# Performance work log

Hardware: AMD Instinct MI355X
Metric: run time of the kernel (lower is better)

## Reference

```python
import jax, jax.numpy as jnp
import numpy as np

B, C, N, HID, OUT = 32768, 128, 12, 200, 2
POOL = 3  # MaxPool2d((1,3), stride=(1,1)) -> N-2 = 10 outputs
EPS = 1e-5


def setup_inputs() -> dict:
    key = jax.random.key(0)
    ks = jax.random.split(key, 18)
    s = 0.05
    return {
        "x": jax.random.normal(ks[0], (B, C, 1, N), jnp.float32),
        "wq": jax.random.normal(ks[1], (C, C), jnp.float32) * s,
        "bq": jax.random.normal(ks[2], (C,), jnp.float32) * s,
        "wk": jax.random.normal(ks[3], (C, C), jnp.float32) * s,
        "bk": jax.random.normal(ks[4], (C,), jnp.float32) * s,
        "wv": jax.random.normal(ks[5], (C, C), jnp.float32) * s,
        "bv": jax.random.normal(ks[6], (C,), jnp.float32) * s,
        "rel_h": jax.random.normal(ks[7], (1, C, N, 1), jnp.float32),
        "rel_w": jax.random.normal(ks[8], (1, C, 1, 1), jnp.float32),
        "bn_gamma": jax.random.uniform(ks[9], (C,), jnp.float32, 0.5, 1.5),
        "bn_beta": jax.random.normal(ks[10], (C,), jnp.float32) * s,
        "bn_mean": jax.random.normal(ks[11], (C,), jnp.float32) * s,
        "bn_var": jax.random.uniform(ks[12], (C,), jnp.float32, 0.5, 1.5),
        "fc1_w": jax.random.normal(ks[13], (HID, (N - POOL + 1) * C), jnp.float32) * s,
        "fc1_b": jax.random.normal(ks[14], (HID,), jnp.float32) * s,
        "fc2_w": jax.random.normal(ks[15], (OUT, HID), jnp.float32) * s,
        "fc2_b": jax.random.normal(ks[16], (OUT,), jnp.float32) * s,
    }


def reference(x, wq, bq, wk, bk, wv, bv, rel_h, rel_w,
              bn_gamma, bn_beta, bn_mean, bn_var,
              fc1_w, fc1_b, fc2_w, fc2_b):
    b, c, w, h = x.shape  # [B, C, 1, 12]
    n = w * h
    xf = x.reshape(b, c, n)  # flatten spatial
    # 1x1 convs == per-position channel mixing
    q = jnp.einsum('oc,bcn->bon', wq, xf) + bq[None, :, None]
    k = jnp.einsum('oc,bcn->bon', wk, xf) + bk[None, :, None]
    v = jnp.einsum('oc,bcn->bon', wv, xf) + bv[None, :, None]
    # content-content: q^T k -> [B, N, N]
    cc = jnp.einsum('bcn,bcm->bnm', q, k)
    # relative-position bias: pos^T q -> [B, N, N]
    pos = (rel_h + rel_w).reshape(c, n)
    cp = jnp.einsum('cn,bcm->bnm', pos, q)
    attn = jax.nn.softmax(cc + cp, axis=-1)
    # out = v @ attn^T : out[b,c,m] = sum_n v[b,c,n] * attn[b,m,n]
    out = jnp.einsum('bcn,bmn->bcm', v, attn)  # [B, C, N]
    # BatchNorm2d (inference) + ReLU
    inv = bn_gamma / jnp.sqrt(bn_var + EPS)
    out = jax.nn.relu(out * inv[None, :, None] + (bn_beta - bn_mean * inv)[None, :, None])
    # MaxPool2d (1,3) stride (1,1) along the N axis
    m = n - POOL + 1
    pooled = jnp.max(jnp.stack([out[..., i:i + m] for i in range(POOL)], axis=0), axis=0)  # [B, C, 10]
    flat = pooled.reshape(b, -1)  # matches torch .view(B,-1) C-major order
    hid = jax.nn.relu(flat @ fc1_w.T + fc1_b)  # dropout = identity (eval)
    return jax.nn.sigmoid(hid @ fc2_w.T + fc2_b)
```

## Files before the change

kernel.cpp:

```cpp
#include <hip/hip_runtime.h>
#include <hip/hip_bf16.h>

#define OFF_G    0u
#define OFF_WVT  32768u
#define OFF_RT   65536u
#define OFF_BNS  71680u
#define OFF_BNB  72192u
#define OFF_FLAG 72704u
#define OFF_W1   72768u
#define OFF_P    605248u

typedef __attribute__((ext_vector_type(8))) unsigned short ushort8_t;
typedef __attribute__((ext_vector_type(8))) __bf16 bf16x8;
typedef __attribute__((ext_vector_type(4))) float f32x4;

static __device__ __forceinline__ float bfbits2f(unsigned short u) {
    return __uint_as_float(((unsigned)u) << 16);
}
static __device__ __forceinline__ unsigned short f2bfbits(float f) {
    __hip_bfloat16 h = __float2bfloat16(f);
    return *(unsigned short*)&h;
}
static __device__ __forceinline__ unsigned pack2bf(float a, float b) {
    return (unsigned)f2bfbits(a) | ((unsigned)f2bfbits(b) << 16);
}
static __device__ __forceinline__ f32x4 mfma16x16x32(ushort8_t a, ushort8_t b, f32x4 c) {
    return __builtin_amdgcn_mfma_f32_16x16x32_bf16(
        __builtin_bit_cast(bf16x8, a), __builtin_bit_cast(bf16x8, b), c, 0, 0, 0);
}

__global__ void setup_kernel(const float* __restrict__ wq, const float* __restrict__ bq,
                             const float* __restrict__ wk,
                             const float* __restrict__ rel_h, const float* __restrict__ rel_w,
                             const float* __restrict__ wv, const float* __restrict__ bvp,
                             const float* __restrict__ gamma, const float* __restrict__ beta,
                             const float* __restrict__ mean, const float* __restrict__ var,
                             const float* __restrict__ fc1w,
                             char* __restrict__ ws)
{
    __hip_bfloat16* GA  = (__hip_bfloat16*)(ws + OFF_G);
    __hip_bfloat16* WA  = (__hip_bfloat16*)(ws + OFF_WVT);
    float*          Rm  = (float*)(ws + OFF_RT);
    float*          BnS = (float*)(ws + OFF_BNS);
    float*          Bi2 = (float*)(ws + OFF_BNB);
    __hip_bfloat16* W1  = (__hip_bfloat16*)(ws + OFF_W1);

    int idx = blockIdx.x * blockDim.x + threadIdx.x;
    if (idx < 16384) {
        int c = idx >> 7, a = idx & 127;
        float s = 0.f;
        for (int o = 0; o < 128; ++o) s += wq[o * 128 + a] * wk[o * 128 + c];
        GA[idx] = __float2bfloat16(s);
    } else if (idx < 32768) {
        int t = idx - 16384;
        int oc = t >> 7;
        float inv = gamma[oc] * rsqrtf(var[oc] + 1e-5f);
        WA[t] = __float2bfloat16(wv[t] * inv);
    } else if (idx < 34304) {
        int t = idx - 32768;
        int c = t / 12, i = t - c * 12;
        float s = 0.f;
        for (int o = 0; o < 128; ++o)
            s += bq[o] * wk[o * 128 + c] + wq[o * 128 + c] * (rel_h[o * 12 + i] + rel_w[o]);
        Rm[t] = s;
    } else if (idx < 34432) {
        int c = idx - 34304;
        float inv = gamma[c] * rsqrtf(var[c] + 1e-5f);
        BnS[c] = inv;
        Bi2[c] = bvp[c] * inv + beta[c] - mean[c] * inv;
    } else if (idx < 300672) {
        int t = idx - 34432;
        int h = t / 1280, k = t - h * 1280;
        W1[t] = (h < 200) ? __float2bfloat16(fc1w[h * 1280 + k])
                          : __float2bfloat16(0.f);
    } else if (idx < 300736) {
        int l = idx - 300672;
        int m = l & 15, g = l >> 4;
        ushort8_t av, bv8;
        for (int j = 0; j < 8; ++j) {
            int k = g * 8 + j;
            float aval = (float)(((m * 5 + k * 3) % 7) - 3);
            float bval = (float)(((k * 11 + m * 2) % 5) - 2);
            av[j]  = (unsigned short)(__float_as_uint(aval) >> 16);
            bv8[j] = (unsigned short)(__float_as_uint(bval) >> 16);
        }
        f32x4 zero = {0.f, 0.f, 0.f, 0.f};
        f32x4 d = mfma16x16x32(av, bv8, zero);
        bool ok = true;
        int col = l & 15;
        for (int r = 0; r < 4; ++r) {
            int row = g * 4 + r;
            float ref = 0.f;
            for (int k = 0; k < 32; ++k)
                ref += (float)(((row * 5 + k * 3) % 7) - 3) *
                       (float)(((k * 11 + col * 2) % 5) - 2);
            if (d[r] != ref) ok = false;
        }
        unsigned long long ball = __ballot(ok ? 1 : 0);
        if (l == 0) *(int*)(ws + OFF_FLAG) = (ball == ~0ull) ? 1 : 0;
    }
}

#define XB_H   0
#define TZY_H  8192
#define PP_H   16384

__launch_bounds__(256, 2)
__global__ void attn_kernel(const float* __restrict__ x,
                            const char* __restrict__ ws,
                            __hip_bfloat16* __restrict__ pooled)
{
    __shared__ __align__(16) char lds[34816];
    unsigned short* LH = (unsigned short*)lds;

    const int tid = threadIdx.x;
    const int w = tid >> 6, l = tid & 63, g = l >> 4, lr = l & 15;

    const unsigned short* GA = (const unsigned short*)(ws + OFF_G);
    const unsigned short* WA = (const unsigned short*)(ws + OFF_WVT);
    const float* Rm  = (const float*)(ws + OFF_RT);
    const float* Bi2 = (const float*)(ws + OFF_BNB);

    ushort8_t gfrag[2][4], wfrag[2][4];
    float bias2v[2], rm[2][4];
    #pragma unroll
    for (int mi = 0; mi < 2; ++mi) {
        int mt = w + mi * 4;
        #pragma unroll
        for (int kt = 0; kt < 4; ++kt) {
            gfrag[mi][kt] = *(const ushort8_t*)(GA + (mt * 16 + lr) * 128 + kt * 32 + g * 8);
            wfrag[mi][kt] = *(const ushort8_t*)(WA + (mt * 16 + lr) * 128 + kt * 32 + g * 8);
        }
        bias2v[mi] = Bi2[mt * 16 + lr];
        #pragma unroll
        for (int r = 0; r < 4; ++r)
            rm[mi][r] = (lr < 12) ? Rm[(mt * 16 + g * 4 + r) * 12 + lr] : 0.f;
    }

    const ushort8_t zero8 = {0, 0, 0, 0, 0, 0, 0, 0};
    {
        int rr = tid >> 4, bb = rr >> 2, sub = rr & 3;
        int n = bb * 16 + 12 + sub;
        *(ushort8_t*)(LH + XB_H + n * 128 + (tid & 15) * 8) = zero8;
    }

    const int c = tid & 127, bh = tid >> 7;

    for (int grp = 0; grp < 4; ++grp) {
        const int b0g = blockIdx.x * 16 + grp * 4;

        #pragma unroll
        for (int b2 = 0; b2 < 2; ++b2) {
            int bl = bh * 2 + b2;
            const float4* xp = (const float4*)(x + ((size_t)(b0g + bl) * 128 + c) * 12);
            float4 xa = xp[0], xb4 = xp[1], xc4 = xp[2];
            float xv[12] = {xa.x, xa.y, xa.z, xa.w, xb4.x, xb4.y, xb4.z, xb4.w,
                            xc4.x, xc4.y, xc4.z, xc4.w};
            #pragma unroll
            for (int i = 0; i < 12; ++i) {
                int n = bl * 16 + i;
                LH[XB_H + n * 128 + (((c >> 3) ^ i) << 3) + (c & 7)] = f2bfbits(xv[i]);
            }
        }
        __syncthreads();

        #pragma unroll
        for (int nt = 0; nt < 4; ++nt) {
            int n = nt * 16 + lr;
            ushort8_t bf[4];
            #pragma unroll
            for (int kt = 0; kt < 4; ++kt)
                bf[kt] = *(const ushort8_t*)(LH + XB_H + n * 128 + ((((kt << 2) + g) ^ lr) << 3));
            #pragma unroll
            for (int mi = 0; mi < 2; ++mi) {
                f32x4 acc = {0.f, 0.f, 0.f, 0.f};
                #pragma unroll
                for (int kt = 0; kt < 4; ++kt) acc = mfma16x16x32(gfrag[mi][kt], bf[kt], acc);
                int ocb = (w + mi * 4) * 16 + g * 4;
                float v0 = acc[0] + rm[mi][0];
                float v1 = acc[1] + rm[mi][1];
                float v2 = acc[2] + rm[mi][2];
                float v3 = acc[3] + rm[mi][3];
                unsigned off = TZY_H + n * 128 + (((ocb >> 3) ^ lr) << 3) + ((g & 1) << 2);
                *(unsigned*)(LH + off)     = pack2bf(v0, v1);
                *(unsigned*)(LH + off + 2) = pack2bf(v2, v3);
            }
        }
        __syncthreads();

        {
            int n = w * 16 + lr;
            f32x4 s = {0.f, 0.f, 0.f, 0.f};
            #pragma unroll
            for (int kt = 0; kt < 4; ++kt) {
                unsigned ch = (((kt << 2) + g) ^ lr) << 3;
                ushort8_t af = *(const ushort8_t*)(LH + TZY_H + n * 128 + ch);
                ushort8_t bf = *(const ushort8_t*)(LH + XB_H + n * 128 + ch);
                s = mfma16x16x32(af, bf, s);
            }
            bool jv = (lr < 12);
            float mx[4], ev[4], sum[4];
            #pragma unroll
            for (int r = 0; r < 4; ++r) mx[r] = jv ? s[r] : -3.0e38f;
            #pragma unroll
            for (int d = 1; d < 16; d <<= 1) {
                #pragma unroll
                for (int r = 0; r < 4; ++r) mx[r] = fmaxf(mx[r], __shfl_xor(mx[r], d));
            }
            #pragma unroll
            for (int r = 0; r < 4; ++r) { ev[r] = jv ? __expf(s[r] - mx[r]) : 0.f; sum[r] = ev[r]; }
            #pragma unroll
            for (int d = 1; d < 16; d <<= 1) {
                #pragma unroll
                for (int r = 0; r < 4; ++r) sum[r] += __shfl_xor(sum[r], d);
            }
            #pragma unroll
            for (int r = 0; r < 4; ++r)
                LH[PP_H + w * 256 + (g * 4 + r) * 16 + lr] = f2bfbits(ev[r] / sum[r]);
        }
        __syncthreads();

        #pragma unroll
        for (int nt = 0; nt < 4; ++nt) {
            int n = nt * 16 + lr;
            ushort8_t bf[4];
            #pragma unroll
            for (int kt = 0; kt < 4; ++kt)
                bf[kt] = *(const ushort8_t*)(LH + XB_H + n * 128 + ((((kt << 2) + g) ^ lr) << 3));
            #pragma unroll
            for (int mi = 0; mi < 2; ++mi) {
                f32x4 acc = {0.f, 0.f, 0.f, 0.f};
                #pragma unroll
                for (int kt = 0; kt < 4; ++kt) acc = mfma16x16x32(wfrag[mi][kt], bf[kt], acc);
                int ocb = (w + mi * 4) * 16 + g * 4;
                #pragma unroll
                for (int r = 0; r < 4; ++r)
                    LH[TZY_H + nt * 2048 + (ocb + r) * 16 + lr] = f2bfbits(acc[r]);
            }
        }
        __syncthreads();

        #pragma unroll
        for (int mi = 0; mi < 2; ++mi) {
            int mt = w + mi * 4;
            float bias = bias2v[mi];
            #pragma unroll
            for (int bb = 0; bb < 4; ++bb) {
                ushort8_t af = (g < 2)
                    ? *(const ushort8_t*)(LH + PP_H + bb * 256 + lr * 16 + g * 8) : zero8;
                ushort8_t bfy = (g < 2)
                    ? *(const ushort8_t*)(LH + TZY_H + bb * 2048 + (mt * 16 + lr) * 16 + g * 8)
                    : zero8;
                f32x4 o = {bias, bias, bias, bias};
                o = mfma16x16x32(af, bfy, o);
                float s0 = __shfl_down(o[0], 16);
                float s1 = __shfl_down(o[1], 16);
                float p0 = fmaxf(fmaxf(fmaxf(o[0], o[1]), o[2]), 0.f);
                float p1 = fmaxf(fmaxf(fmaxf(o[1], o[2]), o[3]), 0.f);
                float p2 = fmaxf(fmaxf(fmaxf(o[2], o[3]), s0), 0.f);
                float p3 = fmaxf(fmaxf(fmaxf(o[3], s0), s1), 0.f);
                unsigned* pw = (unsigned*)((unsigned short*)pooled
                             + (size_t)(b0g + bb) * 1280 + (mt * 16 + lr) * 10 + g * 4);
                if (g < 2) { pw[0] = pack2bf(p0, p1); pw[1] = pack2bf(p2, p3); }
                else if (g == 2) pw[0] = pack2bf(p0, p1);
            }
        }
    }
}

__launch_bounds__(512, 1)
__global__ void fc_kernel(const __hip_bfloat16* __restrict__ pooled_bf,
                          const char* __restrict__ ws,
                          const float* __restrict__ fc1b,
                          const float* __restrict__ fc2w, const float* __restrict__ fc2b,
                          float* __restrict__ out)
{
    __shared__ char smem[54272];
    const int tid = threadIdx.x;
    const int b0  = blockIdx.x * 128;
    const unsigned short* P  = (const unsigned short*)pooled_bf;
    const unsigned short* W1 = (const unsigned short*)(ws + OFF_W1);
    unsigned short* hid = (unsigned short*)smem;
    const int flag = *(const int*)(ws + OFF_FLAG);

    if (flag) {
        const int l = tid & 63, w = tid >> 6;
        const int lrow = l & 15, g = l >> 4;
        f32x4 acc[13];
        #pragma unroll
        for (int nt = 0; nt < 13; ++nt) acc[nt] = (f32x4){0.f, 0.f, 0.f, 0.f};

        const int pr = tid >> 2, pc = tid & 3;
        const size_t pbase = (size_t)(b0 + pr) * 1280 + pc * 8;
        const int i1 = tid, i2 = tid + 512;
        const int h1 = i1 >> 2, c1 = i1 & 3;
        const int h2 = i2 >> 2, c2 = i2 & 3;
        const bool has2 = (i2 < 832);

        ushort8_t pReg, w1a, w1b;
        pReg = *(const ushort8_t*)(P + pbase);
        w1a  = *(const ushort8_t*)(W1 + (size_t)h1 * 1280 + c1 * 8);
        if (has2) w1b = *(const ushort8_t*)(W1 + (size_t)h2 * 1280 + c2 * 8);
        *(ushort8_t*)(smem + tid * 16) = pReg;
        *(ushort8_t*)(smem + 8192 + i1 * 16) = w1a;
        if (has2) *(ushort8_t*)(smem + 8192 + i2 * 16) = w1b;
        __syncthreads();

        int cur = 0;
        for (int ks = 0; ks < 40; ++ks) {
            if (ks + 1 < 40) {
                pReg = *(const ushort8_t*)(P + pbase + (size_t)(ks + 1) * 32);
                w1a  = *(const ushort8_t*)(W1 + (size_t)h1 * 1280 + (ks + 1) * 32 + c1 * 8);
                if (has2) w1b = *(const ushort8_t*)(W1 + (size_t)h2 * 1280 + (ks + 1) * 32 + c2 * 8);
            }
            const unsigned short* Pt = (const unsigned short*)(smem + (cur ? 21504 : 0));
            const unsigned short* Wt = (const unsigned short*)(smem + (cur ? 29696 : 8192));
            ushort8_t A = *(const ushort8_t*)(Pt + (w * 16 + lrow) * 32 + g * 8);
            #pragma unroll
            for (int nt = 0; nt < 13; ++nt) {
                ushort8_t Bf = *(const ushort8_t*)(Wt + (nt * 16 + lrow) * 32 + g * 8);
                acc[nt] = mfma16x16x32(A, Bf, acc[nt]);
            }
            __syncthreads();
            if (ks + 1 < 40) {
                char* dp = smem + ((cur ^ 1) ? 21504 : 0);
                char* dw = smem + ((cur ^ 1) ? 29696 : 8192);
                *(ushort8_t*)(dp + tid * 16) = pReg;
                *(ushort8_t*)(dw + i1 * 16) = w1a;
                if (has2) *(ushort8_t*)(dw + i2 * 16) = w1b;
            }
            __syncthreads();
            cur ^= 1;
        }
        #pragma unroll
        for (int nt = 0; nt < 13; ++nt) {
            int h = nt * 16 + lrow;
            float bias = (h < 200) ? fc1b[h] : 0.f;
            #pragma unroll
            for (int r = 0; r < 4; ++r) {
                float v = fmaxf(acc[nt][r] + bias, 0.f);
                int row = w * 16 + g * 4 + r;
                hid[row * 210 + h] = f2bfbits(v);
            }
        }
    } else {
        for (int i = tid; i < 128 * 200; i += 512) {
            int bb = i / 200, h = i - bb * 200;
            float s = fc1b[h];
            const unsigned short* prow = P + (size_t)(b0 + bb) * 1280;
            const unsigned short* wrow = W1 + (size_t)h * 1280;
            for (int j = 0; j < 1280; ++j)
                s += bfbits2f(prow[j]) * bfbits2f(wrow[j]);
            hid[bb * 210 + h] = f2bfbits(fmaxf(s, 0.f));
        }
    }
    __syncthreads();

    if (tid < 256) {
        int bb = tid >> 1, o = tid & 1;
        float s = fc2b[o];
        const unsigned short* hp = hid + bb * 210;
        const float* wp = fc2w + o * 200;
        #pragma unroll 8
        for (int j = 0; j < 200; ++j)
            s += bfbits2f(hp[j]) * wp[j];
        out[(size_t)(b0 + bb) * 2 + o] = 1.f / (1.f + __expf(-s));
    }
}

extern "C" void kernel_launch(void* const* d_in, const int* in_sizes, int n_in,
                              void* d_out, int out_size, void* d_ws, size_t ws_size,
                              hipStream_t stream)
{
    const float* x     = (const float*)d_in[0];
    const float* wq    = (const float*)d_in[1];
    const float* bq    = (const float*)d_in[2];
    const float* wk    = (const float*)d_in[3];
    const float* wv    = (const float*)d_in[5];
    const float* bv    = (const float*)d_in[6];
    const float* rel_h = (const float*)d_in[7];
    const float* rel_w = (const float*)d_in[8];
    const float* gamma = (const float*)d_in[9];
    const float* beta  = (const float*)d_in[10];
    const float* mean  = (const float*)d_in[11];
    const float* var   = (const float*)d_in[12];
    const float* fc1w  = (const float*)d_in[13];
    const float* fc1b  = (const float*)d_in[14];
    const float* fc2w  = (const float*)d_in[15];
    const float* fc2b  = (const float*)d_in[16];

    char* ws = (char*)d_ws;
    __hip_bfloat16* pooled = (__hip_bfloat16*)(ws + OFF_P);
    float* out = (float*)d_out;

    setup_kernel<<<1175, 256, 0, stream>>>(wq, bq, wk, rel_h, rel_w, wv, bv,
                                           gamma, beta, mean, var, fc1w, ws);
    attn_kernel<<<2048, 256, 0, stream>>>(x, ws, pooled);
    fc_kernel<<<256, 512, 0, stream>>>(pooled, ws, fc1b, fc2w, fc2b, out);
}
```

Measured before the change: 146.9 us.

## Use 512-thread blocks with one output-channel tile per wave, eight batches per group

```diff
diff --git a/kernel.cpp b/kernel.cpp
--- a/kernel.cpp
+++ b/kernel.cpp
@@ -102,15 +102,15 @@
 }
 
 #define XB_H   0
-#define TZY_H  8192
-#define PP_H   16384
-
-__launch_bounds__(256, 2)
+#define TZY_H  16384
+#define PP_H   32768
+
+__launch_bounds__(512, 2)
 __global__ void attn_kernel(const float* __restrict__ x,
                             const char* __restrict__ ws,
                             __hip_bfloat16* __restrict__ pooled)
 {
-    __shared__ __align__(16) char lds[34816];
+    __shared__ __align__(16) char lds[69632];
     unsigned short* LH = (unsigned short*)lds;
 
     const int tid = threadIdx.x;
@@ -121,21 +121,18 @@
     const float* Rm  = (const float*)(ws + OFF_RT);
     const float* Bi2 = (const float*)(ws + OFF_BNB);
 
-    ushort8_t gfrag[2][4], wfrag[2][4];
-    float bias2v[2], rm[2][4];
+    ushort8_t gfrag[4], wfrag[4];
+    float rm[4], b2[8];
     #pragma unroll
-    for (int mi = 0; mi < 2; ++mi) {
-        int mt = w + mi * 4;
-        #pragma unroll
-        for (int kt = 0; kt < 4; ++kt) {
-            gfrag[mi][kt] = *(const ushort8_t*)(GA + (mt * 16 + lr) * 128 + kt * 32 + g * 8);
-            wfrag[mi][kt] = *(const ushort8_t*)(WA + (mt * 16 + lr) * 128 + kt * 32 + g * 8);
-        }
-        bias2v[mi] = Bi2[mt * 16 + lr];
-        #pragma unroll
-        for (int r = 0; r < 4; ++r)
-            rm[mi][r] = (lr < 12) ? Rm[(mt * 16 + g * 4 + r) * 12 + lr] : 0.f;
-    }
+    for (int kt = 0; kt < 4; ++kt) {
+        gfrag[kt] = *(const ushort8_t*)(GA + (w * 16 + lr) * 128 + kt * 32 + g * 8);
+        wfrag[kt] = *(const ushort8_t*)(WA + (w * 16 + lr) * 128 + kt * 32 + g * 8);
+    }
+    #pragma unroll
+    for (int r = 0; r < 4; ++r)
+        rm[r] = (lr < 12) ? Rm[(w * 16 + g * 4 + r) * 12 + lr] : 0.f;
+    #pragma unroll
+    for (int mt = 0; mt < 8; ++mt) b2[mt] = Bi2[mt * 16 + lr];
 
     const ushort8_t zero8 = {0, 0, 0, 0, 0, 0, 0, 0};
     {
@@ -147,11 +144,11 @@
     const int c = tid & 127, bh = tid >> 7;
 
     for (int grp = 0; grp < 4; ++grp) {
-        const int b0g = blockIdx.x * 16 + grp * 4;
-
-        #pragma unroll
-        for (int b2 = 0; b2 < 2; ++b2) {
-            int bl = bh * 2 + b2;
+        const int b0g = blockIdx.x * 32 + grp * 8;
+
+        #pragma unroll
+        for (int b2i = 0; b2i < 2; ++b2i) {
+            int bl = bh * 2 + b2i;
             const float4* xp = (const float4*)(x + ((size_t)(b0g + bl) * 128 + c) * 12);
             float4 xa = xp[0], xb4 = xp[1], xc4 = xp[2];
             float xv[12] = {xa.x, xa.y, xa.z, xa.w, xb4.x, xb4.y, xb4.z, xb4.w,
@@ -165,26 +162,23 @@
         __syncthreads();
 
         #pragma unroll
-        for (int nt = 0; nt < 4; ++nt) {
+        for (int nt = 0; nt < 8; ++nt) {
             int n = nt * 16 + lr;
             ushort8_t bf[4];
             #pragma unroll
             for (int kt = 0; kt < 4; ++kt)
                 bf[kt] = *(const ushort8_t*)(LH + XB_H + n * 128 + ((((kt << 2) + g) ^ lr) << 3));
-            #pragma unroll
-            for (int mi = 0; mi < 2; ++mi) {
-                f32x4 acc = {0.f, 0.f, 0.f, 0.f};
-                #pragma unroll
-                for (int kt = 0; kt < 4; ++kt) acc = mfma16x16x32(gfrag[mi][kt], bf[kt], acc);
-                int ocb = (w + mi * 4) * 16 + g * 4;
-                float v0 = acc[0] + rm[mi][0];
-                float v1 = acc[1] + rm[mi][1];
-                float v2 = acc[2] + rm[mi][2];
-                float v3 = acc[3] + rm[mi][3];
-                unsigned off = TZY_H + n * 128 + (((ocb >> 3) ^ lr) << 3) + ((g & 1) << 2);
-                *(unsigned*)(LH + off)     = pack2bf(v0, v1);
-                *(unsigned*)(LH + off + 2) = pack2bf(v2, v3);
-            }
+            f32x4 acc = {0.f, 0.f, 0.f, 0.f};
+            #pragma unroll
+            for (int kt = 0; kt < 4; ++kt) acc = mfma16x16x32(gfrag[kt], bf[kt], acc);
+            int ocb = w * 16 + g * 4;
+            float v0 = acc[0] + rm[0];
+            float v1 = acc[1] + rm[1];
+            float v2 = acc[2] + rm[2];
+            float v3 = acc[3] + rm[3];
+            unsigned off = TZY_H + n * 128 + (((ocb >> 3) ^ lr) << 3) + ((g & 1) << 2);
+            *(unsigned*)(LH + off)     = pack2bf(v0, v1);
+            *(unsigned*)(LH + off + 2) = pack2bf(v2, v3);
         }
         __syncthreads();
 
@@ -221,38 +215,34 @@
         __syncthreads();
 
         #pragma unroll
-        for (int nt = 0; nt < 4; ++nt) {
+        for (int nt = 0; nt < 8; ++nt) {
             int n = nt * 16 + lr;
             ushort8_t bf[4];
             #pragma unroll
             for (int kt = 0; kt < 4; ++kt)
                 bf[kt] = *(const ushort8_t*)(LH + XB_H + n * 128 + ((((kt << 2) + g) ^ lr) << 3));
-            #pragma unroll
-            for (int mi = 0; mi < 2; ++mi) {
-                f32x4 acc = {0.f, 0.f, 0.f, 0.f};
-                #pragma unroll
-                for (int kt = 0; kt < 4; ++kt) acc = mfma16x16x32(wfrag[mi][kt], bf[kt], acc);
-                int ocb = (w + mi * 4) * 16 + g * 4;
-                #pragma unroll
-                for (int r = 0; r < 4; ++r)
-                    LH[TZY_H + nt * 2048 + (ocb + r) * 16 + lr] = f2bfbits(acc[r]);
-            }
-        }
-        __syncthreads();
-
-        #pragma unroll
-        for (int mi = 0; mi < 2; ++mi) {
-            int mt = w + mi * 4;
-            float bias = bias2v[mi];
-            #pragma unroll
-            for (int bb = 0; bb < 4; ++bb) {
-                ushort8_t af = (g < 2)
-                    ? *(const ushort8_t*)(LH + PP_H + bb * 256 + lr * 16 + g * 8) : zero8;
+            f32x4 acc = {0.f, 0.f, 0.f, 0.f};
+            #pragma unroll
+            for (int kt = 0; kt < 4; ++kt) acc = mfma16x16x32(wfrag[kt], bf[kt], acc);
+            int ocb = w * 16 + g * 4;
+            #pragma unroll
+            for (int r = 0; r < 4; ++r)
+                LH[TZY_H + nt * 2048 + (ocb + r) * 16 + lr] = f2bfbits(acc[r]);
+        }
+        __syncthreads();
+
+        {
+            const int b = b0g + w;
+            ushort8_t paf = (g < 2)
+                ? *(const ushort8_t*)(LH + PP_H + w * 256 + lr * 16 + g * 8) : zero8;
+            #pragma unroll
+            for (int mt = 0; mt < 8; ++mt) {
                 ushort8_t bfy = (g < 2)
-                    ? *(const ushort8_t*)(LH + TZY_H + bb * 2048 + (mt * 16 + lr) * 16 + g * 8)
+                    ? *(const ushort8_t*)(LH + TZY_H + w * 2048 + (mt * 16 + lr) * 16 + g * 8)
                     : zero8;
+                float bias = b2[mt];
                 f32x4 o = {bias, bias, bias, bias};
-                o = mfma16x16x32(af, bfy, o);
+                o = mfma16x16x32(paf, bfy, o);
                 float s0 = __shfl_down(o[0], 16);
                 float s1 = __shfl_down(o[1], 16);
                 float p0 = fmaxf(fmaxf(fmaxf(o[0], o[1]), o[2]), 0.f);
@@ -260,7 +250,7 @@
                 float p2 = fmaxf(fmaxf(fmaxf(o[2], o[3]), s0), 0.f);
                 float p3 = fmaxf(fmaxf(fmaxf(o[3], s0), s1), 0.f);
                 unsigned* pw = (unsigned*)((unsigned short*)pooled
-                             + (size_t)(b0g + bb) * 1280 + (mt * 16 + lr) * 10 + g * 4);
+                             + (size_t)b * 1280 + (mt * 16 + lr) * 10 + g * 4);
                 if (g < 2) { pw[0] = pack2bf(p0, p1); pw[1] = pack2bf(p2, p3); }
                 else if (g == 2) pw[0] = pack2bf(p0, p1);
             }
@@ -395,6 +385,6 @@
 
     setup_kernel<<<1175, 256, 0, stream>>>(wq, bq, wk, rel_h, rel_w, wv, bv,
                                            gamma, beta, mean, var, fc1w, ws);
-    attn_kernel<<<2048, 256, 0, stream>>>(x, ws, pooled);
+    attn_kernel<<<1024, 512, 0, stream>>>(x, ws, pooled);
     fc_kernel<<<256, 512, 0, stream>>>(pooled, ws, fc1b, fc2w, fc2b, out);
 }
```

Measured after the change: 167.3 us. 13.9% more time.
